# Performance work log

Hardware: AMD Instinct MI355X
Metric: run time of the kernel (lower is better)

The kernel has to match this reference:

```python
import jax, jax.numpy as jnp
import numpy as np

B, S, E, KD = 4, 2048, 1024, 1024

def setup_inputs() -> dict:
    key = jax.random.key(0)
    k1, k2, k3, k4 = jax.random.split(key, 4)
    # nn.Linear weights are [out_features, in_features]
    x = jax.random.normal(k1, (B, S, E), dtype=jnp.float32)
    W_q = jax.random.normal(k2, (KD, E), dtype=jnp.float32) * (E ** -0.5)
    W_k = jax.random.normal(k3, (KD, E), dtype=jnp.float32) * (E ** -0.5)
    W_v = jax.random.normal(k4, (E, E), dtype=jnp.float32) * (E ** -0.5)
    return {"x": x, "W_q": W_q, "W_k": W_k, "W_v": W_v}

def reference(x, W_q, W_k, W_v):
    # Projections: y = x @ W.T  (torch Linear convention)
    Q = jnp.einsum('bse,ke->bsk', x, W_q)   # [B,S,KD]
    K = jnp.einsum('bse,ke->bsk', x, W_k)   # [B,S,KD]
    V = jnp.einsum('bse,fe->bsf', x, W_v)   # [B,S,E]
    key_dim = W_q.shape[0]
    scores = jnp.einsum('bqk,bsk->bqs', Q, K) / jnp.sqrt(jnp.asarray(key_dim, x.dtype))
    S_len = x.shape[1]
    causal = jnp.tril(jnp.ones((S_len, S_len), dtype=bool))  # [S,S]
    scores = jnp.where(causal, scores, -jnp.inf)
    weights = jax.nn.softmax(scores, axis=-1)                # [B,S,S]
    out = jnp.einsum('bqs,bsf->bqf', weights, V)             # [B,S,E]
    return out
```

## Files before the change

### kernel.cpp

```cpp
#include <hip/hip_runtime.h>

typedef _Float16 f16;
typedef _Float16 f16x8 __attribute__((ext_vector_type(8)));
typedef float    f32x4 __attribute__((ext_vector_type(4)));

__device__ __forceinline__ void gld_lds16(const void* g, void* l) {
    __builtin_amdgcn_global_load_lds((__attribute__((address_space(1))) void*)g,
                                     (__attribute__((address_space(3))) void*)l,
                                     16, 0, 0);
}

#define BARRIER() do { asm volatile("" ::: "memory"); \
                       __builtin_amdgcn_s_barrier();  \
                       asm volatile("" ::: "memory"); } while (0)

template<bool STG, int VM1, int VM4>
__device__ __forceinline__ void tile256(
    f32x4 (&acc)[8][4],
    const f16* Ak0, const f16* Ak1, const f16* Bk0, const f16* Bk1,
    const f16* gAn, const f16* gBn,
    f16* lAn, f16* lBn,
    int lda, int ldb)
{
    {
        f16x8 a[4], b[4];
        #pragma unroll
        for (int mf = 0; mf < 4; mf++) a[mf] = *(const f16x8*)(Ak0 + mf * 1024);
        #pragma unroll
        for (int nf = 0; nf < 4; nf++) b[nf] = *(const f16x8*)(Bk0 + nf * 1024);
        if (STG) {
            gld_lds16(gBn,                  lBn);
            gld_lds16(gBn + (long)64 * ldb, lBn + 4096);
        }
        BARRIER();
        __builtin_amdgcn_s_setprio(1);
        #pragma unroll
        for (int mf = 0; mf < 4; mf++)
            #pragma unroll
            for (int nf = 0; nf < 4; nf++)
                acc[mf][nf] = __builtin_amdgcn_mfma_f32_16x16x32_f16(
                    a[mf], b[nf], acc[mf][nf], 0, 0, 0);
        __builtin_amdgcn_s_setprio(0);
        if (VM1 == 2)      asm volatile("s_waitcnt vmcnt(2)" ::: "memory");
        else if (VM1 == 0) asm volatile("s_waitcnt vmcnt(0)" ::: "memory");
        BARRIER();
        f16x8 a2[4];
        #pragma unroll
        for (int mf = 0; mf < 4; mf++) a2[mf] = *(const f16x8*)(Ak0 + (mf + 4) * 1024);
        if (STG) {
            gld_lds16(gBn + (long)128 * ldb, lBn + 8192);
            gld_lds16(gBn + (long)192 * ldb, lBn + 12288);
        }
        BARRIER();
        __builtin_amdgcn_s_setprio(1);
        #pragma unroll
        for (int mf = 0; mf < 4; mf++)
            #pragma unroll
            for (int nf = 0; nf < 4; nf++)
                acc[mf + 4][nf] = __builtin_amdgcn_mfma_f32_16x16x32_f16(
                    a2[mf], b[nf], acc[mf + 4][nf], 0, 0, 0);
        __builtin_amdgcn_s_setprio(0);
        BARRIER();
    }
    {
        f16x8 a[4], b[4];
        #pragma unroll
        for (int mf = 0; mf < 4; mf++) a[mf] = *(const f16x8*)(Ak1 + mf * 1024);
        #pragma unroll
        for (int nf = 0; nf < 4; nf++) b[nf] = *(const f16x8*)(Bk1 + nf * 1024);
        if (STG) {
            gld_lds16(gAn,                   lAn);
            gld_lds16(gAn + (long)128 * lda, lAn + 8192);
        }
        BARRIER();
        __builtin_amdgcn_s_setprio(1);
        #pragma unroll
        for (int mf = 0; mf < 4; mf++)
            #pragma unroll
            for (int nf = 0; nf < 4; nf++)
                acc[mf][nf] = __builtin_amdgcn_mfma_f32_16x16x32_f16(
                    a[mf], b[nf], acc[mf][nf], 0, 0, 0);
        __builtin_amdgcn_s_setprio(0);
        BARRIER();
        f16x8 a2[4];
        #pragma unroll
        for (int mf = 0; mf < 4; mf++) a2[mf] = *(const f16x8*)(Ak1 + (mf + 4) * 1024);
        if (STG) {
            gld_lds16(gAn + (long)64 * lda,  lAn + 4096);
            gld_lds16(gAn + (long)192 * lda, lAn + 12288);
        }
        BARRIER();
        __builtin_amdgcn_s_setprio(1);
        #pragma unroll
        for (int mf = 0; mf < 4; mf++)
            #pragma unroll
            for (int nf = 0; nf < 4; nf++)
                acc[mf + 4][nf] = __builtin_amdgcn_mfma_f32_16x16x32_f16(
                    a2[mf], b[nf], acc[mf + 4][nf], 0, 0, 0);
        __builtin_amdgcn_s_setprio(0);
        if (VM4 == 2)      asm volatile("s_waitcnt vmcnt(2)" ::: "memory");
        else if (VM4 == 0) asm volatile("s_waitcnt vmcnt(0)" ::: "memory");
        BARRIER();
    }
}

__global__ void __launch_bounds__(512, 2)
gemm256_k1024(const f16* __restrict__ A, const f16* __restrict__ B,
              f16* __restrict__ C, int lda, int ldb, int ldc)
{
    const int m  = (int)blockIdx.x;
    const int L  = (m & 7) * 32 + (m >> 3);
    const int i0 = (L >> 3) * 256;
    const int j0 = (L & 7) * 256;

    __shared__ f16 Lds[2 * 32768] __attribute__((aligned(16)));

    const int tid  = threadIdx.x;
    const int lane = tid & 63;
    const int wave = tid >> 6;
    const int wm = wave >> 2, wn = wave & 3;
    const int row16 = lane & 15, quad = lane >> 4;
    const int swz = row16 & 7;

    const int c0 = (quad ^ swz) * 8;
    const int c1 = ((quad + 4) ^ swz) * 8;
    const f16* A0k0 = Lds + (wm * 128 + row16) * 64 + c0;
    const f16* A0k1 = Lds + (wm * 128 + row16) * 64 + c1;
    const f16* B0k0 = Lds + 16384 + (wn * 64 + row16) * 64 + c0;
    const f16* B0k1 = Lds + 16384 + (wn * 64 + row16) * 64 + c1;

    const int srow = tid >> 3;
    const int scol = ((tid & 7) ^ (srow & 7)) * 8;
    const f16* gA = A + (long)(i0 + srow) * lda + scol;
    const f16* gB = B + (long)(j0 + srow) * ldb + scol;
    f16* lA0 = Lds + tid * 8;
    f16* lB0 = Lds + 16384 + tid * 8;
    f16* lA1 = Lds + 32768 + tid * 8;
    f16* lB1 = Lds + 32768 + 16384 + tid * 8;

    gld_lds16(gB,                   lB0);
    gld_lds16(gB + (long)64 * ldb,  lB0 + 4096);
    gld_lds16(gB + (long)128 * ldb, lB0 + 8192);
    gld_lds16(gB + (long)192 * ldb, lB0 + 12288);
    gld_lds16(gA,                   lA0);
    gld_lds16(gA + (long)128 * lda, lA0 + 8192);
    gld_lds16(gA + (long)64 * lda,  lA0 + 4096);
    gld_lds16(gA + (long)192 * lda, lA0 + 12288);

    f32x4 acc[8][4] = {};

    asm volatile("s_waitcnt vmcnt(2)" ::: "memory");
    BARRIER();

    for (int t = 0; t < 14; t += 2) {
        tile256<true, 2, 2>(acc, A0k0, A0k1, B0k0, B0k1,
                            gA + (t + 1) * 64, gB + (t + 1) * 64,
                            lA1, lB1, lda, ldb);
        tile256<true, 2, 2>(acc, A0k0 + 32768, A0k1 + 32768,
                            B0k0 + 32768, B0k1 + 32768,
                            gA + (t + 2) * 64, gB + (t + 2) * 64,
                            lA0, lB0, lda, ldb);
    }
    tile256<true, 2, 2>(acc, A0k0, A0k1, B0k0, B0k1,
                        gA + 15 * 64, gB + 15 * 64, lA1, lB1, lda, ldb);
    tile256<false, 0, -1>(acc, A0k0 + 32768, A0k1 + 32768,
                          B0k0 + 32768, B0k1 + 32768,
                          nullptr, nullptr, nullptr, nullptr, lda, ldb);

    #pragma unroll
    for (int mf = 0; mf < 8; mf++) {
        const int r0 = i0 + wm * 128 + mf * 16 + quad * 4;
        #pragma unroll
        for (int nf = 0; nf < 4; nf++) {
            const int c = j0 + wn * 64 + nf * 16 + row16;
            #pragma unroll
            for (int r = 0; r < 4; r++)
                C[(long)(r0 + r) * ldc + c] = (f16)acc[mf][nf][r];
        }
    }
}

template<typename OutT>
__device__ __forceinline__ void gemm128_body(
    const f16* __restrict__ A, const f16* __restrict__ B, OutT* __restrict__ C,
    int lda, int ldb, int ldc, int Keff, float scale, int i0, int j0)
{
    __shared__ f16 As[128 * 64] __attribute__((aligned(16)));
    __shared__ f16 Bs[64 * 64]  __attribute__((aligned(16)));

    const int tid  = threadIdx.x;
    const int lane = tid & 63;
    const int wave = tid >> 6;
    const int row16 = lane & 15;
    const int quad  = lane >> 4;
    const int swz   = row16 & 7;
    const int wr = (wave >> 1) * 64;
    const int wc = (wave & 1) * 32;

    const int srow = tid >> 3;
    const int scol = ((tid & 7) ^ (srow & 7)) * 8;
    const f16* gA = A + (long)(i0 + srow) * lda + scol;
    const f16* gB = B + (long)(j0 + srow) * ldb + scol;
    f16* lA = As + tid * 8;
    f16* lB = Bs + tid * 8;

    f32x4 acc[4][2] = {};

    for (int k0 = 0; k0 < Keff; k0 += 64) {
        gld_lds16(gA + k0,                  lA);
        gld_lds16(gA + k0 + (long)32 * lda, lA + 32 * 64);
        gld_lds16(gA + k0 + (long)64 * lda, lA + 64 * 64);
        gld_lds16(gA + k0 + (long)96 * lda, lA + 96 * 64);
        gld_lds16(gB + k0,                  lB);
        gld_lds16(gB + k0 + (long)32 * ldb, lB + 32 * 64);
        __syncthreads();

        #pragma unroll
        for (int kk = 0; kk < 2; kk++) {
            f16x8 af[4], bf[2];
            #pragma unroll
            for (int t = 0; t < 4; t++)
                af[t] = *(const f16x8*)(As + (wr + t * 16 + row16) * 64
                                           + (((kk * 4 + quad) ^ swz) * 8));
            #pragma unroll
            for (int t = 0; t < 2; t++)
                bf[t] = *(const f16x8*)(Bs + (wc + t * 16 + row16) * 64
                                           + (((kk * 4 + quad) ^ swz) * 8));
            #pragma unroll
            for (int mt = 0; mt < 4; mt++)
                #pragma unroll
                for (int nt = 0; nt < 2; nt++)
                    acc[mt][nt] = __builtin_amdgcn_mfma_f32_16x16x32_f16(
                        af[mt], bf[nt], acc[mt][nt], 0, 0, 0);
        }
        __syncthreads();
    }

    #pragma unroll
    for (int mt = 0; mt < 4; mt++) {
        const int r0 = i0 + wr + mt * 16 + quad * 4;
        #pragma unroll
        for (int nt = 0; nt < 2; nt++) {
            const int c = j0 + wc + nt * 16 + row16;
            #pragma unroll
            for (int r = 0; r < 4; r++)
                C[(long)(r0 + r) * ldc + c] = (OutT)(acc[mt][nt][r] * scale);
        }
    }
}

__global__ void __launch_bounds__(256)
gemm_vt_sc(const f16* __restrict__ xh, const f16* __restrict__ wvh,
           const f16* __restrict__ QKh, f16* __restrict__ Vt,
           f16* __restrict__ Sc)
{
    const int blk = (int)blockIdx.x;
    if (blk < 1024) {
        const int L = (blk & 7) * 128 + (blk >> 3);
        const int j = L >> 3;
        const int i = L & 7;
        gemm128_body<f16>(wvh, xh, Vt, 1024, 1024, 8192, 1024, 1.f,
                          i * 128, j * 64);
    } else {
        const int m = blk - 1024;
        const int L = (m & 7) * 136 + (m >> 3);
        const int z = L / 272;
        const int r = L - z * 272;
        int y = 0;
        while ((y + 1) * (y + 2) <= r) y++;
        const int x = r - y * (y + 1);
        const long off = (long)z * (2048L * 2048);
        gemm128_body<f16>(QKh + off, QKh + 1024 + off, Sc + off,
                          2048, 2048, 2048, 1024, 0.03125f, y * 128, x * 64);
    }
}

__global__ void __launch_bounds__(256)
gemm_pv(const f16* __restrict__ Sc, const f16* __restrict__ Vt,
        float* __restrict__ out)
{
    const int n  = (int)blockIdx.x;
    const int by = 15 - (n >> 6);
    const int rem = n & 63;
    const int x  = rem >> 2;
    const int z  = rem & 3;
    const int i0 = by * 128;
    const int j0 = x * 64;
    const int Keff = i0 + 128;
    gemm128_body<float>(Sc + (long)z * (2048L * 2048),
                        Vt + (long)z * 2048,
                        out + (long)z * (2048L * 1024),
                        2048, 8192, 1024, Keff, 1.f, i0, j0);
}

__global__ void __launch_bounds__(256)
softmax_causal(f16* __restrict__ Sc)
{
    const int S = 2048;
    const long rowg = blockIdx.x;
    const long b = rowg >> 11;
    const int  i = (int)(rowg & 2047);
    f16* row = Sc + ((b * S + i) * (long)S);
    const int L = ((i >> 7) + 1) << 7;

    const int tid = threadIdx.x;
    const int c0  = tid * 8;
    const int lane = tid & 63, wave = tid >> 6;
    const bool act = c0 < L;

    float v[8];
    float m = -3.4e38f;
    if (act) {
        f16x8 in = *(const f16x8*)(row + c0);
        #pragma unroll
        for (int j = 0; j < 8; j++) {
            const bool ok = (c0 + j) <= i;
            v[j] = ok ? (float)in[j] : -3.4e38f;
            m = fmaxf(m, v[j]);
        }
    }
    #pragma unroll
    for (int off = 32; off > 0; off >>= 1)
        m = fmaxf(m, __shfl_down(m, off, 64));
    __shared__ float redm[4];
    if (lane == 0) redm[wave] = m;
    __syncthreads();
    const float m0 = fmaxf(fmaxf(redm[0], redm[1]), fmaxf(redm[2], redm[3]));

    float e[8];
    float s = 0.f;
    if (act) {
        #pragma unroll
        for (int j = 0; j < 8; j++) {
            const bool ok = (c0 + j) <= i;
            e[j] = ok ? __expf(v[j] - m0) : 0.f;
            s += e[j];
        }
    }
    #pragma unroll
    for (int off = 32; off > 0; off >>= 1)
        s += __shfl_down(s, off, 64);
    __shared__ float reds[4];
    if (lane == 0) reds[wave] = s;
    __syncthreads();
    const float inv = 1.f / (reds[0] + reds[1] + reds[2] + reds[3]);

    if (act) {
        f16x8 o;
        #pragma unroll
        for (int j = 0; j < 8; j++) o[j] = (f16)(e[j] * inv);
        *(f16x8*)(row + c0) = o;
    }
}

__global__ void __launch_bounds__(256)
convert_all(const float* __restrict__ x, const float* __restrict__ Wq,
            const float* __restrict__ Wk, const float* __restrict__ Wv,
            f16* __restrict__ xh, f16* __restrict__ wh)
{
    const long blk = blockIdx.x;
    const float* src;
    f16* dst;
    long base;
    if (blk < 4096)      { src = x;  dst = xh;                    base = blk * 2048; }
    else if (blk < 4608) { src = Wq; dst = wh;                    base = (blk - 4096) * 2048; }
    else if (blk < 5120) { src = Wk; dst = wh + 1024L * 1024;     base = (blk - 4608) * 2048; }
    else                 { src = Wv; dst = wh + 2L * 1024 * 1024; base = (blk - 5120) * 2048; }
    const long i = base + (long)threadIdx.x * 8;
    f32x4 a = *(const f32x4*)(src + i);
    f32x4 b = *(const f32x4*)(src + i + 4);
    f16x8 o;
    o[0] = (f16)a[0]; o[1] = (f16)a[1]; o[2] = (f16)a[2]; o[3] = (f16)a[3];
    o[4] = (f16)b[0]; o[5] = (f16)b[1]; o[6] = (f16)b[2]; o[7] = (f16)b[3];
    *(f16x8*)(dst + i) = o;
}

extern "C" void kernel_launch(void* const* d_in, const int* in_sizes, int n_in,
                              void* d_out, int out_size, void* d_ws, size_t ws_size,
                              hipStream_t stream)
{
    (void)in_sizes; (void)n_in; (void)out_size; (void)ws_size;
    const float* x  = (const float*)d_in[0];
    const float* Wq = (const float*)d_in[1];
    const float* Wk = (const float*)d_in[2];
    const float* Wv = (const float*)d_in[3];
    float* out = (float*)d_out;

    const long NX = 4L * 2048 * 1024;
    const long NW = 1024L * 1024;

    char* p = (char*)d_ws;
    f16* xh  = (f16*)p; p += NX * 2;
    f16* wh  = (f16*)p; p += 3 * NW * 2;
    f16* QKh = (f16*)p; p += 2 * NX * 2;
    f16* Vt  = (f16*)p; p += NX * 2;
    f16* Sc  = (f16*)p; p += 4L * 2048 * 2048 * 2;
    f16* wvh = wh + 2L * NW;

    convert_all<<<5632, 256, 0, stream>>>(x, Wq, Wk, Wv, xh, wh);

    gemm256_k1024<<<256, 512, 0, stream>>>(
        xh, wh, QKh, 1024, 1024, 2048);

    gemm_vt_sc<<<2112, 256, 0, stream>>>(xh, wvh, QKh, Vt, Sc);

    softmax_causal<<<4 * 2048, 256, 0, stream>>>(Sc);

    gemm_pv<<<1024, 256, 0, stream>>>(Sc, Vt, out);
}
```

Measured before the change: 219.6 us.

## Fuse all attention stages into one persistent cooperative kernel with grid syncs

Replaces the five separate launches (convert, QK projection, V/score GEMMs, softmax, PV) with a single cooperative kernel of 256 blocks of 512 threads. Stages are separated by grid.sync, and each block runs two independent 256-thread halves that process 128x64 GEMM tiles and softmax rows in a strided loop. The aim is to remove kernel launch gaps and tail effects between stages. In exchange, parallelism is fixed at 256 resident blocks, which lowers occupancy for the small-tile GEMMs and adds grid-wide barrier cost. If the cooperative launch fails, it falls back to the old multi-kernel path.

```diff
diff --git a/kernel.cpp b/kernel.cpp
--- a/kernel.cpp
+++ b/kernel.cpp
@@ -1,4 +1,7 @@
 #include <hip/hip_runtime.h>
+#include <hip/hip_cooperative_groups.h>
+
+namespace cg = cooperative_groups;
 
 typedef _Float16 f16;
 typedef _Float16 f16x8 __attribute__((ext_vector_type(8)));
@@ -18,9 +21,7 @@
 __device__ __forceinline__ void tile256(
     f32x4 (&acc)[8][4],
     const f16* Ak0, const f16* Ak1, const f16* Bk0, const f16* Bk1,
-    const f16* gAn, const f16* gBn,
-    f16* lAn, f16* lBn,
-    int lda, int ldb)
+    const f16* gAn, const f16* gBn, f16* lAn, f16* lBn, int lda, int ldb)
 {
     {
         f16x8 a[4], b[4];
@@ -104,18 +105,14 @@
     }
 }
 
-__global__ void __launch_bounds__(512, 2)
-gemm256_k1024(const f16* __restrict__ A, const f16* __restrict__ B,
-              f16* __restrict__ C, int lda, int ldb, int ldc)
-{
-    const int m  = (int)blockIdx.x;
+__device__ __forceinline__ void qk256(
+    const f16* __restrict__ A, const f16* __restrict__ B, f16* __restrict__ C,
+    int lda, int ldb, int ldc, f16* Lds, int tid, int m)
+{
     const int L  = (m & 7) * 32 + (m >> 3);
     const int i0 = (L >> 3) * 256;
     const int j0 = (L & 7) * 256;
 
-    __shared__ f16 Lds[2 * 32768] __attribute__((aligned(16)));
-
-    const int tid  = threadIdx.x;
     const int lane = tid & 63;
     const int wave = tid >> 6;
     const int wm = wave >> 2, wn = wave & 3;
@@ -181,28 +178,28 @@
 }
 
 template<typename OutT>
-__device__ __forceinline__ void gemm128_body(
+__device__ __forceinline__ void gemm128_half(
     const f16* __restrict__ A, const f16* __restrict__ B, OutT* __restrict__ C,
-    int lda, int ldb, int ldc, int Keff, float scale, int i0, int j0)
-{
-    __shared__ f16 As[128 * 64] __attribute__((aligned(16)));
-    __shared__ f16 Bs[64 * 64]  __attribute__((aligned(16)));
-
-    const int tid  = threadIdx.x;
-    const int lane = tid & 63;
-    const int wave = tid >> 6;
+    int lda, int ldb, int ldc, int Keff, float scale, int i0, int j0,
+    f16* lds, int t)
+{
+    f16* As = lds;
+    f16* Bs = lds + 128 * 64;
+
+    const int lane = t & 63;
+    const int wave = t >> 6;
     const int row16 = lane & 15;
     const int quad  = lane >> 4;
     const int swz   = row16 & 7;
     const int wr = (wave >> 1) * 64;
     const int wc = (wave & 1) * 32;
 
-    const int srow = tid >> 3;
-    const int scol = ((tid & 7) ^ (srow & 7)) * 8;
+    const int srow = t >> 3;
+    const int scol = ((t & 7) ^ (srow & 7)) * 8;
     const f16* gA = A + (long)(i0 + srow) * lda + scol;
     const f16* gB = B + (long)(j0 + srow) * ldb + scol;
-    f16* lA = As + tid * 8;
-    f16* lB = Bs + tid * 8;
+    f16* lA = As + t * 8;
+    f16* lB = Bs + t * 8;
 
     f32x4 acc[4][2] = {};
 
@@ -219,12 +216,12 @@
         for (int kk = 0; kk < 2; kk++) {
             f16x8 af[4], bf[2];
             #pragma unroll
-            for (int t = 0; t < 4; t++)
-                af[t] = *(const f16x8*)(As + (wr + t * 16 + row16) * 64
+            for (int u = 0; u < 4; u++)
+                af[u] = *(const f16x8*)(As + (wr + u * 16 + row16) * 64
                                            + (((kk * 4 + quad) ^ swz) * 8));
             #pragma unroll
-            for (int t = 0; t < 2; t++)
-                bf[t] = *(const f16x8*)(Bs + (wc + t * 16 + row16) * 64
+            for (int u = 0; u < 2; u++)
+                bf[u] = *(const f16x8*)(Bs + (wc + u * 16 + row16) * 64
                                            + (((kk * 4 + quad) ^ swz) * 8));
             #pragma unroll
             for (int mt = 0; mt < 4; mt++)
@@ -249,29 +246,190 @@
     }
 }
 
+__global__ void __launch_bounds__(512, 2)
+attn_all(const float* __restrict__ x, const float* __restrict__ Wq,
+         const float* __restrict__ Wk, const float* __restrict__ Wv,
+         f16* __restrict__ xh, f16* __restrict__ wh,
+         f16* __restrict__ QKh, f16* __restrict__ Vt,
+         f16* __restrict__ Sc, float* __restrict__ out)
+{
+    cg::grid_group grid = cg::this_grid();
+    __shared__ f16 Lds[65536] __attribute__((aligned(16)));
+
+    const int bid = (int)blockIdx.x;
+    const int tid = (int)threadIdx.x;
+    const int h   = tid >> 8;
+    const int t   = tid & 255;
+
+    {
+        const long base = (long)bid * 512 + tid;
+        for (long c = base; c < 1048576; c += 131072) {
+            const long i = c * 8;
+            f32x4 a = *(const f32x4*)(x + i);
+            f32x4 b = *(const f32x4*)(x + i + 4);
+            f16x8 o;
+            o[0]=(f16)a[0]; o[1]=(f16)a[1]; o[2]=(f16)a[2]; o[3]=(f16)a[3];
+            o[4]=(f16)b[0]; o[5]=(f16)b[1]; o[6]=(f16)b[2]; o[7]=(f16)b[3];
+            *(f16x8*)(xh + i) = o;
+        }
+        for (long c = base; c < 393216; c += 131072) {
+            const float* src;
+            long off;
+            if (c < 131072)      { src = Wq; off = c * 8; }
+            else if (c < 262144) { src = Wk; off = (c - 131072) * 8; }
+            else                 { src = Wv; off = (c - 262144) * 8; }
+            f32x4 a = *(const f32x4*)(src + off);
+            f32x4 b = *(const f32x4*)(src + off + 4);
+            f16x8 o;
+            o[0]=(f16)a[0]; o[1]=(f16)a[1]; o[2]=(f16)a[2]; o[3]=(f16)a[3];
+            o[4]=(f16)b[0]; o[5]=(f16)b[1]; o[6]=(f16)b[2]; o[7]=(f16)b[3];
+            *(f16x8*)(wh + c * 8) = o;
+        }
+    }
+    grid.sync();
+
+    qk256(xh, wh, QKh, 1024, 1024, 2048, Lds, tid, bid);
+    grid.sync();
+
+    {
+        const int xcd = bid & 7;
+        const int le  = (bid >> 3) * 2 + h;
+        f16* myLds = Lds + h * 12288;
+        const int trips = (le < 8) ? 5 : 4;
+        for (int i = 0; i < trips; i++) {
+            const int v = le + 64 * i;
+            if (v < 128) {
+                const int L = xcd * 128 + v;
+                gemm128_half<f16>(wh + 2L * 1048576, xh, Vt,
+                                  1024, 1024, 8192, 1024, 1.f,
+                                  (L & 7) * 128, (L >> 3) * 64, myLds, t);
+            } else {
+                const int L = xcd * 136 + (v - 128);
+                const int z = L / 272;
+                const int r = L - z * 272;
+                int y = 0;
+                while ((y + 1) * (y + 2) <= r) y++;
+                const int xx = r - y * (y + 1);
+                const long off = (long)z * (2048L * 2048);
+                gemm128_half<f16>(QKh + off, QKh + 1024 + off, Sc + off,
+                                  2048, 2048, 2048, 1024, 0.03125f,
+                                  y * 128, xx * 64, myLds, t);
+            }
+            __syncthreads();
+        }
+    }
+    grid.sync();
+
+    {
+        float* redm = (float*)Lds + h * 16;
+        float* reds = redm + 8;
+        for (int rp = 0; rp < 16; rp++) {
+            const long rowg = (long)rp * 512 + bid * 2 + h;
+            const long b = rowg >> 11;
+            const int  i = (int)(rowg & 2047);
+            f16* row = Sc + ((b * 2048 + i) * 2048L);
+            const int Lp = ((i >> 7) + 1) << 7;
+            const int c0 = t * 8;
+            const int lane = t & 63, wv = t >> 6;
+            const bool act = c0 < Lp;
+
+            float v[8];
+            float m = -3.4e38f;
+            if (act) {
+                f16x8 in = *(const f16x8*)(row + c0);
+                #pragma unroll
+                for (int j = 0; j < 8; j++) {
+                    const bool ok = (c0 + j) <= i;
+                    v[j] = ok ? (float)in[j] : -3.4e38f;
+                    m = fmaxf(m, v[j]);
+                }
+            }
+            #pragma unroll
+            for (int off = 32; off > 0; off >>= 1)
+                m = fmaxf(m, __shfl_down(m, off, 64));
+            if (lane == 0) redm[wv] = m;
+            __syncthreads();
+            const float m0 = fmaxf(fmaxf(redm[0], redm[1]),
+                                   fmaxf(redm[2], redm[3]));
+
+            float e[8];
+            float s = 0.f;
+            if (act) {
+                #pragma unroll
+                for (int j = 0; j < 8; j++) {
+                    const bool ok = (c0 + j) <= i;
+                    e[j] = ok ? __expf(v[j] - m0) : 0.f;
+                    s += e[j];
+                }
+            }
+            #pragma unroll
+            for (int off = 32; off > 0; off >>= 1)
+                s += __shfl_down(s, off, 64);
+            if (lane == 0) reds[wv] = s;
+            __syncthreads();
+            const float inv = 1.f / (reds[0] + reds[1] + reds[2] + reds[3]);
+
+            if (act) {
+                f16x8 o;
+                #pragma unroll
+                for (int j = 0; j < 8; j++) o[j] = (f16)(e[j] * inv);
+                *(f16x8*)(row + c0) = o;
+            }
+            __syncthreads();
+        }
+    }
+    grid.sync();
+
+    {
+        f16* myLds = Lds + h * 12288;
+        for (int it = 0; it < 2; it++) {
+            const int p = it ? 511 - bid : bid;
+            const int g = p >> 5;
+            const int by = 15 - g;
+            const int rem = p & 31;
+            const int x2 = rem >> 2, z = rem & 3;
+            const int i0 = by * 128;
+            gemm128_half<float>(Sc + (long)z * (2048L * 2048),
+                                Vt + (long)z * 2048,
+                                out + (long)z * (2048L * 1024),
+                                2048, 8192, 1024, i0 + 128, 1.f,
+                                i0, (x2 * 2 + h) * 64, myLds, t);
+            __syncthreads();
+        }
+    }
+}
+
+__global__ void __launch_bounds__(512, 2)
+gemm256_k1024(const f16* __restrict__ A, const f16* __restrict__ B,
+              f16* __restrict__ C, int lda, int ldb, int ldc)
+{
+    __shared__ f16 L[65536] __attribute__((aligned(16)));
+    qk256(A, B, C, lda, ldb, ldc, L, (int)threadIdx.x, (int)blockIdx.x);
+}
+
 __global__ void __launch_bounds__(256)
 gemm_vt_sc(const f16* __restrict__ xh, const f16* __restrict__ wvh,
            const f16* __restrict__ QKh, f16* __restrict__ Vt,
            f16* __restrict__ Sc)
 {
+    __shared__ f16 L[12288] __attribute__((aligned(16)));
     const int blk = (int)blockIdx.x;
     if (blk < 1024) {
-        const int L = (blk & 7) * 128 + (blk >> 3);
-        const int j = L >> 3;
-        const int i = L & 7;
-        gemm128_body<f16>(wvh, xh, Vt, 1024, 1024, 8192, 1024, 1.f,
-                          i * 128, j * 64);
+        const int Lx = (blk & 7) * 128 + (blk >> 3);
+        gemm128_half<f16>(wvh, xh, Vt, 1024, 1024, 8192, 1024, 1.f,
+                          (Lx & 7) * 128, (Lx >> 3) * 64, L, (int)threadIdx.x);
     } else {
         const int m = blk - 1024;
-        const int L = (m & 7) * 136 + (m >> 3);
-        const int z = L / 272;
-        const int r = L - z * 272;
+        const int Lx = (m & 7) * 136 + (m >> 3);
+        const int z = Lx / 272;
+        const int r = Lx - z * 272;
         int y = 0;
         while ((y + 1) * (y + 2) <= r) y++;
-        const int x = r - y * (y + 1);
+        const int xx = r - y * (y + 1);
         const long off = (long)z * (2048L * 2048);
-        gemm128_body<f16>(QKh + off, QKh + 1024 + off, Sc + off,
-                          2048, 2048, 2048, 1024, 0.03125f, y * 128, x * 64);
+        gemm128_half<f16>(QKh + off, QKh + 1024 + off, Sc + off,
+                          2048, 2048, 2048, 1024, 0.03125f,
+                          y * 128, xx * 64, L, (int)threadIdx.x);
     }
 }
 
@@ -279,18 +437,18 @@
 gemm_pv(const f16* __restrict__ Sc, const f16* __restrict__ Vt,
         float* __restrict__ out)
 {
+    __shared__ f16 L[12288] __attribute__((aligned(16)));
     const int n  = (int)blockIdx.x;
     const int by = 15 - (n >> 6);
     const int rem = n & 63;
     const int x  = rem >> 2;
     const int z  = rem & 3;
     const int i0 = by * 128;
-    const int j0 = x * 64;
-    const int Keff = i0 + 128;
-    gemm128_body<float>(Sc + (long)z * (2048L * 2048),
+    gemm128_half<float>(Sc + (long)z * (2048L * 2048),
                         Vt + (long)z * 2048,
                         out + (long)z * (2048L * 1024),
-                        2048, 8192, 1024, Keff, 1.f, i0, j0);
+                        2048, 8192, 1024, i0 + 128, 1.f,
+                        i0, x * 64, L, (int)threadIdx.x);
 }
 
 __global__ void __launch_bounds__(256)
@@ -397,14 +555,18 @@
     f16* Sc  = (f16*)p; p += 4L * 2048 * 2048 * 2;
     f16* wvh = wh + 2L * NW;
 
-    convert_all<<<5632, 256, 0, stream>>>(x, Wq, Wk, Wv, xh, wh);
-
-    gemm256_k1024<<<256, 512, 0, stream>>>(
-        xh, wh, QKh, 1024, 1024, 2048);
-
-    gemm_vt_sc<<<2112, 256, 0, stream>>>(xh, wvh, QKh, Vt, Sc);
-
-    softmax_causal<<<4 * 2048, 256, 0, stream>>>(Sc);
-
-    gemm_pv<<<1024, 256, 0, stream>>>(Sc, Vt, out);
-}
+    void* args[] = { (void*)&x, (void*)&Wq, (void*)&Wk, (void*)&Wv,
+                     (void*)&xh, (void*)&wh, (void*)&QKh, (void*)&Vt,
+                     (void*)&Sc, (void*)&out };
+    hipError_t err = hipLaunchCooperativeKernel(
+        (const void*)attn_all, dim3(256), dim3(512), args, 0, stream);
+
+    if (err != hipSuccess) {
+        (void)hipGetLastError();
+        convert_all<<<5632, 256, 0, stream>>>(x, Wq, Wk, Wv, xh, wh);
+        gemm256_k1024<<<256, 512, 0, stream>>>(xh, wh, QKh, 1024, 1024, 2048);
+        gemm_vt_sc<<<2112, 256, 0, stream>>>(xh, wvh, QKh, Vt, Sc);
+        softmax_causal<<<4 * 2048, 256, 0, stream>>>(Sc);
+        gemm_pv<<<1024, 256, 0, stream>>>(Sc, Vt, out);
+    }
+}
```

After: 409.2 us. +86.3%, slower.
